# Performance work log

Measured on AMD Instinct MI355X. Metric: run time of the kernel, lower is better.

Reference implementation:

```python
import jax, jax.numpy as jnp
import numpy as np

# Architecture constants (from module defaults)
D, H, DH, P, G, DEPTH, M, NCLS = 192, 3, 64, 16, 14, 12, 128, 1000  # M = feature_map_dim // 2
EXITS = (4, 8, 12)
TEMP = 1.0 / np.sqrt(DH)  # Favor softmax_temp = 1/sqrt(d_head)
EPS_ATTN = 1e-6           # fast_transformers LinearAttention eps
LN_EPS = 1e-5


def ln(x, g, b):
    mu = x.mean(-1, keepdims=True)
    var = ((x - mu) ** 2).mean(-1, keepdims=True)
    return (x - mu) * jax.lax.rsqrt(var + LN_EPS) * g + b


def favor(x, omega):
    # FAVOR+ positive random features for the softmax kernel.
    # x: [B,L,H,DH], omega: [DH,M] -> phi: [B,L,H,2M]
    xs = x * np.float32(np.sqrt(TEMP))
    off = 0.5 * (xs * xs).sum(-1, keepdims=True)
    u = jnp.einsum('blhd,dm->blhm', xs, omega)
    phi = jnp.concatenate([jnp.exp(u - off), jnp.exp(-u - off)], axis=-1)
    return phi * np.float32(1.0 / np.sqrt(2 * M))


def forward(x, patch_w, patch_b, pe_ln_g, pe_ln_b, cls_token, pos_embed,
            Wq, bq, Wk, bk, Wv, bv, Wo, bo,
            ln1_g, ln1_b, ln2_g, ln2_b, lnb_g, lnb_b,
            W1, b1, W2, b2, omega, head_w, head_b):
    B = x.shape[0]
    # Patch embedding: Conv2d(k=16, s=16) == blocked einsum
    xp = x.reshape(B, 3, G, P, G, P)
    tok = jnp.einsum('bchpwq,dcpq->bhwd', xp, patch_w).reshape(B, G * G, D) + patch_b
    tok = ln(tok, pe_ln_g, pe_ln_b)  # PatchEmbed.norm (norm_layer=LayerNorm)
    tok = jnp.concatenate([jnp.broadcast_to(cls_token, (B, 1, D)), tok], axis=1) + pos_embed
    xc = tok  # [B, 197, D]
    outs = []
    for i in range(DEPTH):
        # --- linear (FAVOR) attention ---
        q = (xc @ Wq[i].T + bq[i]).reshape(B, -1, H, DH)
        k = (xc @ Wk[i].T + bk[i]).reshape(B, -1, H, DH)
        v = (xc @ Wv[i].T + bv[i]).reshape(B, -1, H, DH)
        Qp = favor(q, omega[i])
        Kp = favor(k, omega[i])
        KV = jnp.einsum('bshm,bshd->bhmd', Kp, v)
        Z = 1.0 / (jnp.einsum('blhm,bhm->blh', Qp, Kp.sum(axis=1)) + EPS_ATTN)
        attn = jnp.einsum('blhm,bhmd,blh->blhd', Qp, KV, Z).reshape(B, -1, D)
        # fast_transformers TransformerEncoderLayer (post-norm style)
        xc = xc + attn @ Wo[i].T + bo[i]
        y = xc = ln(xc, ln1_g[i], ln1_b[i])
        y = jax.nn.relu(y @ W1[i].T + b1[i]) @ W2[i].T + b2[i]
        xc = ln(xc + y, ln2_g[i], ln2_b[i])
        # per-block TransformerEncoder final norm (builder final_normalization)
        xc = ln(xc, lnb_g[i], lnb_b[i])
        if (i + 1) in EXITS:
            j = EXITS.index(i + 1)
            z = xc.mean(axis=1)  # AdaptiveAvgPool1d(1) over sequence
            outs.append(z @ head_w[j].T + head_b[j])
    return tuple(outs)


def setup_inputs() -> dict:
    key = jax.random.key(0)
    ks = iter(jax.random.split(key, 32))
    n = lambda shape, s=0.02: jax.random.normal(next(ks), shape, jnp.float32) * s
    return dict(
        x=jax.random.normal(next(ks), (64, 3, 224, 224), jnp.float32),
        patch_w=n((D, 3, P, P)), patch_b=jnp.zeros((D,), jnp.float32),
        pe_ln_g=jnp.ones((D,), jnp.float32), pe_ln_b=jnp.zeros((D,), jnp.float32),
        cls_token=n((1, 1, D)), pos_embed=n((1, G * G + 1, D)),
        Wq=n((DEPTH, D, D)), bq=jnp.zeros((DEPTH, D), jnp.float32),
        Wk=n((DEPTH, D, D)), bk=jnp.zeros((DEPTH, D), jnp.float32),
        Wv=n((DEPTH, D, D)), bv=jnp.zeros((DEPTH, D), jnp.float32),
        Wo=n((DEPTH, D, D)), bo=jnp.zeros((DEPTH, D), jnp.float32),
        ln1_g=jnp.ones((DEPTH, D), jnp.float32), ln1_b=jnp.zeros((DEPTH, D), jnp.float32),
        ln2_g=jnp.ones((DEPTH, D), jnp.float32), ln2_b=jnp.zeros((DEPTH, D), jnp.float32),
        lnb_g=jnp.ones((DEPTH, D), jnp.float32), lnb_b=jnp.zeros((DEPTH, D), jnp.float32),
        W1=n((DEPTH, 4 * D, D)), b1=jnp.zeros((DEPTH, 4 * D), jnp.float32),
        W2=n((DEPTH, D, 4 * D)), b2=jnp.zeros((DEPTH, D), jnp.float32),
        omega=jax.random.normal(next(ks), (DEPTH, DH, M), jnp.float32),
        head_w=n((len(EXITS), NCLS, D)), head_b=jnp.zeros((len(EXITS), NCLS), jnp.float32),
    )


def reference(x, patch_w, patch_b, pe_ln_g, pe_ln_b, cls_token, pos_embed,
              Wq, bq, Wk, bk, Wv, bv, Wo, bo,
              ln1_g, ln1_b, ln2_g, ln2_b, lnb_g, lnb_b,
              W1, b1, W2, b2, omega, head_w, head_b):
    return forward(x, patch_w, patch_b, pe_ln_g, pe_ln_b, cls_token, pos_embed,
                   Wq, bq, Wk, bk, Wv, bv, Wo, bo,
                   ln1_g, ln1_b, ln2_g, ln2_b, lnb_g, lnb_b,
                   W1, b1, W2, b2, omega, head_w, head_b)
```

## Files before the change

### kernel.cpp

```cpp
#include <hip/hip_runtime.h>
#include <math.h>

#define BB     64
#define LLEN   197
#define BLROWS 12608
#define MPAD   12672
#define DMODEL 192
#define NHEAD  3
#define DHEAD  64
#define M2FEAT 256
#define FFDIM  768
#define NDEPTH 12
#define NCLS   1000
#define NPATCH 196
#define BPROWS 12544
#define KPATCH 768
#define PHIRS  264
#define PHTRS  40
#define VLT    208

#define MODE_PLAIN 0
#define MODE_RELU  1
#define MODE_QKV   2

typedef unsigned short ushort;
typedef __attribute__((ext_vector_type(8))) short bf16x8;
typedef __attribute__((ext_vector_type(4))) float floatx4;
typedef __attribute__((ext_vector_type(4))) short short4v;

__device__ __forceinline__ float wave_reduce_sum(float v) {
#pragma unroll
  for (int s = 32; s > 0; s >>= 1) v += __shfl_xor(v, s, 64);
  return v;
}
__device__ __forceinline__ ushort f2bf(float f) {
  unsigned u = __float_as_uint(f);
  return (ushort)((u + 0x7fffu + ((u >> 16) & 1u)) >> 16);
}
__device__ __forceinline__ float bf2f(ushort u) {
  return __uint_as_float(((unsigned)u) << 16);
}
__device__ __forceinline__ void gll16(const ushort* g, ushort* l) {
  __builtin_amdgcn_global_load_lds(
      (const __attribute__((address_space(1))) void*)g,
      (__attribute__((address_space(3))) void*)l, 16, 0, 0);
}

__global__ void zero_buf(uint4* __restrict__ p, int n16) {
  const int i = blockIdx.x * 256 + threadIdx.x;
  if (i < n16) p[i] = uint4{0, 0, 0, 0};
}

__global__ __launch_bounds__(256) void gemm_bf2(
    const ushort* __restrict__ A, int lda,
    const ushort* __restrict__ W, int ldw,
    const float* __restrict__ bias,
    ushort* __restrict__ C, int ldc, ushort* __restrict__ Vt,
    int Kdim, int mode)
{
  __shared__ __align__(16) ushort As[2][128 * 64];
  __shared__ __align__(16) ushort Ws[2][64 * 64];
  const int tid = threadIdx.x;
  const int bm = blockIdx.x, bn = blockIdx.y;
  const int wave = tid >> 6, lane = tid & 63;
  const int wm = (wave >> 1) * 64, wn = (wave & 1) * 32;
  const int quad = lane >> 4, l16 = lane & 15;
  const int srow = lane >> 3;
  const int scol = ((lane & 7) ^ srow) * 8;
  const ushort* Ap = A + (size_t)(bm * 128) * lda;
  const ushort* Wp = W + (size_t)(bn * 64) * ldw;
  floatx4 acc[4][2] = {};
  const int nT = Kdim >> 6;
#pragma unroll
  for (int t = 0; t < 4; ++t) {
    const int rb = (t * 4 + wave) * 8;
    gll16(Ap + (size_t)(rb + srow) * lda + scol, &As[0][rb * 64]);
  }
#pragma unroll
  for (int t = 0; t < 2; ++t) {
    const int rb = (t * 4 + wave) * 8;
    gll16(Wp + (size_t)(rb + srow) * ldw + scol, &Ws[0][rb * 64]);
  }
  for (int kt = 0; kt < nT; ++kt) {
    const int cur = kt & 1;
    __syncthreads();
    if (kt + 1 < nT) {
      const int kk = (kt + 1) * 64, nxt = cur ^ 1;
#pragma unroll
      for (int t = 0; t < 4; ++t) {
        const int rb = (t * 4 + wave) * 8;
        gll16(Ap + (size_t)(rb + srow) * lda + kk + scol, &As[nxt][rb * 64]);
      }
#pragma unroll
      for (int t = 0; t < 2; ++t) {
        const int rb = (t * 4 + wave) * 8;
        gll16(Wp + (size_t)(rb + srow) * ldw + kk + scol, &Ws[nxt][rb * 64]);
      }
    }
#pragma unroll
    for (int ks = 0; ks < 2; ++ks) {
      bf16x8 af[4], bf[2];
#pragma unroll
      for (int i = 0; i < 4; ++i) {
        const int ra = wm + i * 16 + l16;
        af[i] = *(const bf16x8*)&As[cur][ra * 64 + ((((ks << 2) | quad) ^ (ra & 7)) * 8)];
      }
#pragma unroll
      for (int j = 0; j < 2; ++j) {
        const int rw = wn + j * 16 + l16;
        bf[j] = *(const bf16x8*)&Ws[cur][rw * 64 + ((((ks << 2) | quad) ^ (rw & 7)) * 8)];
      }
#pragma unroll
      for (int i = 0; i < 4; ++i)
#pragma unroll
        for (int j = 0; j < 2; ++j)
          acc[i][j] = __builtin_amdgcn_mfma_f32_16x16x32_bf16(af[i], bf[j], acc[i][j], 0, 0, 0);
    }
  }
  if (mode == MODE_QKV) {
#pragma unroll
    for (int i = 0; i < 4; ++i)
#pragma unroll
      for (int r = 0; r < 4; ++r) {
        const int grow = bm * 128 + wm + i * 16 + quad * 4 + r;
        const int bidx = grow / 197;
        const int lloc = grow - bidx * 197;
#pragma unroll
        for (int j = 0; j < 2; ++j) {
          const int col = bn * 64 + wn + j * 16 + l16;
          const float o = acc[i][j][r] + bias[col];
          if (col < 384) {
            C[(size_t)grow * ldc + col] = f2bf(o);
          } else if (grow < BLROWS) {
            const int h = (col - 384) >> 6, d = (col - 384) & 63;
            Vt[((size_t)(bidx * 3 + h) * 64 + d) * VLT + lloc] = f2bf(o);
          }
        }
      }
  } else {
#pragma unroll
    for (int j = 0; j < 2; ++j) {
      const int col = bn * 64 + wn + j * 16 + l16;
      const float bv = bias[col];
#pragma unroll
      for (int i = 0; i < 4; ++i)
#pragma unroll
        for (int r = 0; r < 4; ++r) {
          const int grow = bm * 128 + wm + i * 16 + quad * 4 + r;
          float o = acc[i][j][r] + bv;
          if (mode == MODE_RELU) o = fmaxf(o, 0.f);
          C[(size_t)grow * ldc + col] = f2bf(o);
        }
    }
  }
}

__global__ __launch_bounds__(256) void gemm_ln(
    const ushort* __restrict__ A, int lda,
    const ushort* __restrict__ W, int ldw,
    const float* __restrict__ bias,
    ushort* __restrict__ XC,
    const float* __restrict__ ga, const float* __restrict__ ba,
    const float* __restrict__ gb, const float* __restrict__ bb,
    int Kdim, int dln)
{
  __shared__ __align__(16) ushort As[2][32 * 64];
  __shared__ __align__(16) ushort Ws[2][192 * 64];
  __shared__ float p1s[2][32], p1q[2][32], p2s[2][32], p2q[2][32];
  const int tid = threadIdx.x;
  const int bm = blockIdx.x;
  const int wave = tid >> 6, lane = tid & 63;
  const int rg = wave >> 1, cg = wave & 1;
  const int quad = lane >> 4, l16 = lane & 15;
  const int srow = lane >> 3;
  const int scol = ((lane & 7) ^ srow) * 8;
  const ushort* Ap = A + (size_t)(bm * 32) * lda;
  floatx4 acc[6] = {};
  const int nT = Kdim >> 6;
  gll16(Ap + (size_t)(wave * 8 + srow) * lda + scol, &As[0][wave * 8 * 64]);
#pragma unroll
  for (int t = 0; t < 6; ++t) {
    const int rb = (t * 4 + wave) * 8;
    gll16(W + (size_t)(rb + srow) * ldw + scol, &Ws[0][rb * 64]);
  }
  for (int kt = 0; kt < nT; ++kt) {
    const int cur = kt & 1;
    __syncthreads();
    if (kt + 1 < nT) {
      const int kk = (kt + 1) * 64, nxt = cur ^ 1;
      gll16(Ap + (size_t)(wave * 8 + srow) * lda + kk + scol, &As[nxt][wave * 8 * 64]);
#pragma unroll
      for (int t = 0; t < 6; ++t) {
        const int rb = (t * 4 + wave) * 8;
        gll16(W + (size_t)(rb + srow) * ldw + kk + scol, &Ws[nxt][rb * 64]);
      }
    }
#pragma unroll
    for (int ks = 0; ks < 2; ++ks) {
      const int ra = rg * 16 + l16;
      const bf16x8 af = *(const bf16x8*)&As[cur][ra * 64 + ((((ks << 2) | quad) ^ (ra & 7)) * 8)];
#pragma unroll
      for (int j = 0; j < 6; ++j) {
        const int rw = (cg * 6 + j) * 16 + l16;
        const bf16x8 bf = *(const bf16x8*)&Ws[cur][rw * 64 + ((((ks << 2) | quad) ^ (rw & 7)) * 8)];
        acc[j] = __builtin_amdgcn_mfma_f32_16x16x32_bf16(af, bf, acc[j], 0, 0, 0);
      }
    }
  }
  float xr[4][6];
#pragma unroll
  for (int r = 0; r < 4; ++r) {
    const int rloc = rg * 16 + quad * 4 + r;
    const int row = bm * 32 + rloc;
    const ushort* xp = XC + (size_t)row * DMODEL;
    float s = 0.f, sq = 0.f;
#pragma unroll
    for (int j = 0; j < 6; ++j) {
      const int col = (cg * 6 + j) * 16 + l16;
      const float o = acc[j][r] + bias[col] + bf2f(xp[col]);
      xr[r][j] = o; s += o; sq += o * o;
    }
#pragma unroll
    for (int m = 1; m < 16; m <<= 1) {
      s += __shfl_xor(s, m, 64); sq += __shfl_xor(sq, m, 64);
    }
    if (l16 == 0) { p1s[cg][rloc] = s; p1q[cg][rloc] = sq; }
  }
  __syncthreads();
#pragma unroll
  for (int r = 0; r < 4; ++r) {
    const int rloc = rg * 16 + quad * 4 + r;
    const float s = p1s[0][rloc] + p1s[1][rloc];
    const float sq = p1q[0][rloc] + p1q[1][rloc];
    const float mu = s * (1.f / 192.f);
    const float var = sq * (1.f / 192.f) - mu * mu;
    const float rs = rsqrtf(var + 1e-5f);
#pragma unroll
    for (int j = 0; j < 6; ++j) {
      const int col = (cg * 6 + j) * 16 + l16;
      xr[r][j] = (xr[r][j] - mu) * rs * ga[col] + ba[col];
    }
  }
  if (dln) {
#pragma unroll
    for (int r = 0; r < 4; ++r) {
      const int rloc = rg * 16 + quad * 4 + r;
      float s = 0.f, sq = 0.f;
#pragma unroll
      for (int j = 0; j < 6; ++j) { s += xr[r][j]; sq += xr[r][j] * xr[r][j]; }
#pragma unroll
      for (int m = 1; m < 16; m <<= 1) {
        s += __shfl_xor(s, m, 64); sq += __shfl_xor(sq, m, 64);
      }
      if (l16 == 0) { p2s[cg][rloc] = s; p2q[cg][rloc] = sq; }
    }
    __syncthreads();
#pragma unroll
    for (int r = 0; r < 4; ++r) {
      const int rloc = rg * 16 + quad * 4 + r;
      const float s = p2s[0][rloc] + p2s[1][rloc];
      const float sq = p2q[0][rloc] + p2q[1][rloc];
      const float mu = s * (1.f / 192.f);
      const float var = sq * (1.f / 192.f) - mu * mu;
      const float rs = rsqrtf(var + 1e-5f);
#pragma unroll
      for (int j = 0; j < 6; ++j) {
        const int col = (cg * 6 + j) * 16 + l16;
        xr[r][j] = (xr[r][j] - mu) * rs * gb[col] + bb[col];
      }
    }
  }
#pragma unroll
  for (int r = 0; r < 4; ++r) {
    const int row = bm * 32 + rg * 16 + quad * 4 + r;
    ushort* xp = XC + (size_t)row * DMODEL;
#pragma unroll
    for (int j = 0; j < 6; ++j) xp[(cg * 6 + j) * 16 + l16] = f2bf(xr[r][j]);
  }
}

__global__ __launch_bounds__(256) void kv_fused(
    const ushort* __restrict__ qkv, const ushort* __restrict__ OmT,
    const ushort* __restrict__ Vt, ushort* __restrict__ KVt)
{
  __shared__ __align__(16) ushort Ks[32 * 64];
  __shared__ __align__(16) ushort Om[64 * 64];
  __shared__ __align__(16) ushort PhT[128 * PHTRS];
  __shared__ __align__(16) ushort Vts[2][64 * 32];
  __shared__ __align__(16) ushort Vcst[16 * 32];
  __shared__ float offs[32];
  const int tid = threadIdx.x;
  const int bh = blockIdx.x, mh = blockIdx.y;
  const int b = bh / 3, h = bh - b * 3;
  const int wave = tid >> 6, lane = tid & 63;
  const int quad = lane >> 4, l16 = lane & 15;
  const int lr8 = lane >> 3, g8 = lane & 7;
  const int lr4 = lane >> 2, g4 = lane & 3;
#pragma unroll
  for (int t = 0; t < 2; ++t) {
    const int rb = (t * 4 + wave) * 8;
    const int row = rb + lr8;
    gll16(OmT + (size_t)(mh * 64 + row) * 64 + ((g8 ^ (row & 7)) * 8), &Om[rb * 64]);
  }
  {
    const int rowK = wave * 8 + lr8;
    gll16(qkv + (size_t)(b * 197 + rowK) * 576 + 192 + h * 64 + ((g8 ^ (rowK & 7)) * 8),
          &Ks[wave * 8 * 64]);
    const int rowV = wave * 16 + lr4;
    gll16(Vt + ((size_t)bh * 64 + rowV) * VLT + ((g4 ^ (rowV & 3)) * 8),
          &Vts[0][wave * 16 * 32]);
  }
  for (int e = tid; e < 16 * 32; e += 256) Vcst[e] = (e < 32) ? 0x3F80 : 0;
  floatx4 acc[2][5] = {};
  for (int c = 0; c < 7; ++c) {
    const int l0 = c * 32;
    const int cur = c & 1;
    __syncthreads();
    if (tid < 64) {
      const int row = tid >> 1, half = tid & 1;
      float s = 0.f;
#pragma unroll
      for (int t = 0; t < 4; ++t) {
        bf16x8 v8 = *(const bf16x8*)&Ks[row * 64 + (((half * 4 + t) ^ (row & 7)) * 8)];
#pragma unroll
        for (int q = 0; q < 8; ++q) { float xv = bf2f((ushort)v8[q]); s += xv * xv; }
      }
      s += __shfl_xor(s, 1, 64);
      if (half == 0) offs[row] = 0.0625f * s;
    }
    floatx4 ui[2] = {};
#pragma unroll
    for (int ksb = 0; ksb < 2; ++ksb) {
      bf16x8 af[2], bfm;
#pragma unroll
      for (int i = 0; i < 2; ++i) {
        const int row = i * 16 + l16;
        af[i] = *(const bf16x8*)&Ks[row * 64 + (((quad + (ksb << 2)) ^ (row & 7)) * 8)];
      }
      {
        const int row = wave * 16 + l16;
        bfm = *(const bf16x8*)&Om[row * 64 + (((quad + (ksb << 2)) ^ (row & 7)) * 8)];
      }
#pragma unroll
      for (int i = 0; i < 2; ++i)
        ui[i] = __builtin_amdgcn_mfma_f32_16x16x32_bf16(af[i], bfm, ui[i], 0, 0, 0);
    }
    __syncthreads();
    {
      const int mloc = wave * 16 + l16;
#pragma unroll
      for (int i = 0; i < 2; ++i) {
#pragma unroll
        for (int r = 0; r < 4; ++r) {
          const int ll = i * 16 + quad * 4 + r;
          float ep = 0.f, em = 0.f;
          if (l0 + ll < 197) {
            const float off = offs[ll];
            const float u = ui[i][r];
            ep = __expf(u - off) * 0.0625f;
            em = __expf(-u - off) * 0.0625f;
          }
          PhT[mloc * PHTRS + ll] = f2bf(ep);
          PhT[(64 + mloc) * PHTRS + ll] = f2bf(em);
        }
      }
    }
    if (c + 1 < 7) {
      const int rowK = wave * 8 + lr8;
      const int lK = (c + 1) * 32 + rowK;
      gll16(qkv + (size_t)(b * 197 + lK) * 576 + 192 + h * 64 + ((g8 ^ (rowK & 7)) * 8),
            &Ks[wave * 8 * 64]);
      const int rowV = wave * 16 + lr4;
      gll16(Vt + ((size_t)bh * 64 + rowV) * VLT + (c + 1) * 32 + ((g4 ^ (rowV & 3)) * 8),
            &Vts[cur ^ 1][wave * 16 * 32]);
    }
    __syncthreads();
    bf16x8 af[2], bf[5];
#pragma unroll
    for (int i = 0; i < 2; ++i)
      af[i] = *(const bf16x8*)&PhT[(wave * 32 + i * 16 + l16) * PHTRS + quad * 8];
#pragma unroll
    for (int j = 0; j < 4; ++j) {
      const int row = j * 16 + l16;
      bf[j] = *(const bf16x8*)&Vts[cur][row * 32 + ((quad ^ (row & 3)) * 8)];
    }
    bf[4] = *(const bf16x8*)&Vcst[l16 * 32 + quad * 8];
#pragma unroll
    for (int i = 0; i < 2; ++i)
#pragma unroll
      for (int j = 0; j < 5; ++j)
        acc[i][j] = __builtin_amdgcn_mfma_f32_16x16x32_bf16(af[i], bf[j], acc[i][j], 0, 0, 0);
  }
#pragma unroll
  for (int i = 0; i < 2; ++i) {
    const int prow0 = wave * 32 + i * 16 + quad * 4;
    const int f0 = (prow0 < 64) ? (mh * 64 + prow0) : (128 + mh * 64 + prow0 - 64);
#pragma unroll
    for (int j = 0; j < 5; ++j) {
      const int d = j * 16 + l16;
      short4v pk;
#pragma unroll
      for (int r = 0; r < 4; ++r) pk[r] = (short)f2bf(acc[i][j][r]);
      *(short4v*)(KVt + ((size_t)bh * 80 + d) * 256 + f0) = pk;
    }
  }
}

__global__ __launch_bounds__(256) void attn_fused(
    const ushort* __restrict__ qkv, const ushort* __restrict__ OmT,
    const ushort* __restrict__ KVt, ushort* __restrict__ OUT)
{
  __shared__ __align__(16) ushort Phi[64 * PHIRS];
  __shared__ __align__(16) ushort Bs[2][80 * 32];
  __shared__ float offs[64];
  __shared__ float zs[64];
  ushort* Qs = Phi;
  ushort* Om = Phi + 64 * 64;
  const int tid = threadIdx.x;
  const int bx = blockIdx.x, bh = blockIdx.y;
  const int b = bh / 3, h = bh - b * 3;
  const int wave = tid >> 6, lane = tid & 63;
  const int quad = lane >> 4, l16 = lane & 15;
  const int lr8 = lane >> 3, g8 = lane & 7;
  const int lr4 = lane >> 2, g4 = lane & 3;
#pragma unroll
  for (int t = 0; t < 2; ++t) {
    const int rb = wave * 16 + t * 8;
    const int row = rb + lr8;
    const int l = bx * 64 + row;
    gll16(qkv + (size_t)(b * 197 + l) * 576 + h * 64 + ((g8 ^ (row & 7)) * 8), &Qs[rb * 64]);
  }
#pragma unroll
  for (int t = 0; t < 4; ++t) {
    const int rb = wave * 32 + t * 8;
    const int row = rb + lr8;
    gll16(OmT + (size_t)row * 64 + ((g8 ^ (row & 7)) * 8), &Om[rb * 64]);
  }
  __syncthreads();
  if (tid < 128) {
    const int row = tid >> 1, half = tid & 1;
    float s = 0.f;
#pragma unroll
    for (int t = 0; t < 4; ++t) {
      bf16x8 v8 = *(const bf16x8*)&Qs[row * 64 + (((half * 4 + t) ^ (row & 7)) * 8)];
#pragma unroll
      for (int q = 0; q < 8; ++q) { float xv = bf2f((ushort)v8[q]); s += xv * xv; }
    }
    s += __shfl_xor(s, 1, 64);
    if (half == 0) offs[row] = 0.0625f * s;
  }
  floatx4 uacc[8] = {};
#pragma unroll
  for (int ksb = 0; ksb < 2; ++ksb) {
    bf16x8 af, bf[8];
    {
      const int row = wave * 16 + l16;
      af = *(const bf16x8*)&Qs[row * 64 + (((quad + (ksb << 2)) ^ (row & 7)) * 8)];
    }
#pragma unroll
    for (int j = 0; j < 8; ++j) {
      const int row = j * 16 + l16;
      bf[j] = *(const bf16x8*)&Om[row * 64 + (((quad + (ksb << 2)) ^ (row & 7)) * 8)];
    }
#pragma unroll
    for (int j = 0; j < 8; ++j)
      uacc[j] = __builtin_amdgcn_mfma_f32_16x16x32_bf16(af, bf[j], uacc[j], 0, 0, 0);
  }
  __syncthreads();
#pragma unroll
  for (int r = 0; r < 4; ++r) {
    const int l = wave * 16 + quad * 4 + r;
    const float off = offs[l];
#pragma unroll
    for (int j = 0; j < 8; ++j) {
      const int m = j * 16 + l16;
      const float u = uacc[j][r];
      Phi[l * PHIRS + m]       = f2bf(__expf(u - off)  * 0.0625f);
      Phi[l * PHIRS + m + 128] = f2bf(__expf(-u - off) * 0.0625f);
    }
  }
  const ushort* Bp = KVt + (size_t)bh * 80 * 256;
  {
    const int row = wave * 16 + lr4;
    gll16(Bp + (size_t)row * 256 + ((g4 ^ (row & 3)) * 8), &Bs[0][wave * 16 * 32]);
    if (wave == 0)
      gll16(Bp + (size_t)(64 + lr4) * 256 + ((g4 ^ (lr4 & 3)) * 8), &Bs[0][64 * 32]);
  }
  floatx4 acc[5] = {};
  for (int c = 0; c < 8; ++c) {
    const int cur = c & 1;
    __syncthreads();
    if (c + 1 < 8) {
      const int m0 = (c + 1) * 32, nxt = cur ^ 1;
      const int row = wave * 16 + lr4;
      gll16(Bp + (size_t)row * 256 + m0 + ((g4 ^ (row & 3)) * 8), &Bs[nxt][wave * 16 * 32]);
      if (wave == 0)
        gll16(Bp + (size_t)(64 + lr4) * 256 + m0 + ((g4 ^ (lr4 & 3)) * 8), &Bs[nxt][64 * 32]);
    }
    const int m0 = c * 32;
    bf16x8 af, bf[5];
    af = *(const bf16x8*)&Phi[(wave * 16 + l16) * PHIRS + m0 + quad * 8];
#pragma unroll
    for (int j = 0; j < 5; ++j) {
      const int row = j * 16 + l16;
      bf[j] = *(const bf16x8*)&Bs[cur][row * 32 + ((quad ^ (row & 3)) * 8)];
    }
#pragma unroll
    for (int j = 0; j < 5; ++j)
      acc[j] = __builtin_amdgcn_mfma_f32_16x16x32_bf16(af, bf[j], acc[j], 0, 0, 0);
  }
  if (l16 == 0) {
#pragma unroll
    for (int r = 0; r < 4; ++r)
      zs[wave * 16 + quad * 4 + r] = acc[4][r];
  }
  __syncthreads();
#pragma unroll
  for (int r = 0; r < 4; ++r) {
    const int ll = wave * 16 + quad * 4 + r;
    const int l = bx * 64 + ll;
    if (l >= 197) continue;
    const float z = 1.f / (zs[ll] + 1e-6f);
#pragma unroll
    for (int j = 0; j < 4; ++j)
      OUT[(size_t)(b * 197 + l) * 192 + h * 64 + j * 16 + l16] =
          f2bf(acc[j][r] * z);
  }
}

__global__ void conv_qkv(const float* __restrict__ Wq, const float* __restrict__ Wk,
                         const float* __restrict__ Wv, const float* __restrict__ bq,
                         const float* __restrict__ bk, const float* __restrict__ bv,
                         ushort* __restrict__ dst, float* __restrict__ bdst) {
  const int l = blockIdx.y;
  const int e = blockIdx.x * 256 + threadIdx.x;
  const int n = e / 192, k = e - n * 192;
  const float* src;
  if (n < 192)      src = Wq + (size_t)l * 36864 + n * 192;
  else if (n < 384) src = Wk + (size_t)l * 36864 + (n - 192) * 192;
  else              src = Wv + (size_t)l * 36864 + (n - 384) * 192;
  dst[(size_t)l * 640 * 192 + e] = f2bf(src[k]);
  if (e < 576) {
    float bvv;
    if (e < 192)      bvv = bq[l * 192 + e];
    else if (e < 384) bvv = bk[l * 192 + e - 192];
    else              bvv = bv[l * 192 + e - 384];
    bdst[l * 576 + e] = bvv;
  }
}

__global__ void conv_pad(const float* __restrict__ src, ushort* __restrict__ dst,
                         int NK, int padNK) {
  const int l = blockIdx.y;
  const int e = blockIdx.x * 256 + threadIdx.x;
  if (e < NK) dst[(size_t)l * padNK + e] = f2bf(src[(size_t)l * NK + e]);
}

__global__ void conv_omt(const float* __restrict__ om, ushort* __restrict__ dst) {
  const int l = blockIdx.y;
  const int e = blockIdx.x * 256 + threadIdx.x;
  const int m = e >> 6, d = e & 63;
  dst[(size_t)l * 8192 + e] = f2bf(0.35355339059327379f * om[(size_t)l * 8192 + d * 128 + m]);
}

__global__ __launch_bounds__(256) void im2col_kernel(
    const float* __restrict__ X, ushort* __restrict__ Apd)
{
  const int bp = blockIdx.x;
  const int b = bp / NPATCH, p = bp - b * NPATCH;
  const int gh = p / 14, gw = p - gh * 14;
  for (int e = threadIdx.x; e < KPATCH; e += 256) {
    const int c = e >> 8, rem = e & 255, ph = rem >> 4, pw = rem & 15;
    Apd[(size_t)bp * KPATCH + e] =
        f2bf(X[((size_t)(b * 3 + c) * 224 + gh * 16 + ph) * 224 + gw * 16 + pw]);
  }
}

__global__ __launch_bounds__(256) void assemble_kernel(
    const ushort* __restrict__ TK, const float* __restrict__ g,
    const float* __restrict__ bt, const float* __restrict__ cls,
    const float* __restrict__ pos, ushort* __restrict__ XC)
{
  const int w = threadIdx.x >> 6, lane = threadIdx.x & 63;
  const int row = blockIdx.x * 4 + w;
  const int b = row / LLEN, l = row - b * LLEN;
  float o0, o1, o2;
  if (l == 0) {
    o0 = cls[lane]; o1 = cls[lane + 64]; o2 = cls[lane + 128];
  } else {
    const ushort* tp = TK + (size_t)(b * NPATCH + l - 1) * DMODEL;
    const float x0 = bf2f(tp[lane]), x1 = bf2f(tp[lane + 64]), x2 = bf2f(tp[lane + 128]);
    const float s  = wave_reduce_sum(x0 + x1 + x2);
    const float sq = wave_reduce_sum(x0 * x0 + x1 * x1 + x2 * x2);
    const float mu = s * (1.f / 192.f);
    const float var = sq * (1.f / 192.f) - mu * mu;
    const float rs = rsqrtf(var + 1e-5f);
    o0 = (x0 - mu) * rs * g[lane]       + bt[lane];
    o1 = (x1 - mu) * rs * g[lane + 64]  + bt[lane + 64];
    o2 = (x2 - mu) * rs * g[lane + 128] + bt[lane + 128];
  }
  o0 += pos[l * DMODEL + lane];
  o1 += pos[l * DMODEL + lane + 64];
  o2 += pos[l * DMODEL + lane + 128];
  ushort* xp = XC + (size_t)row * DMODEL;
  xp[lane] = f2bf(o0); xp[lane + 64] = f2bf(o1); xp[lane + 128] = f2bf(o2);
}

__global__ __launch_bounds__(256) void head_kernel(
    const ushort* __restrict__ XC, const float* __restrict__ HW,
    const float* __restrict__ HB, float* __restrict__ OUTp)
{
  __shared__ float zsh[DMODEL];
  const int b = blockIdx.y;
  const int tid = threadIdx.x;
  const int wave = tid >> 6, lane = tid & 63;
  if (wave < 3) {
    const int d = wave * 64 + lane;
    const ushort* xp = XC + (size_t)b * LLEN * DMODEL + d;
    float s = 0.f;
#pragma unroll 4
    for (int l = 0; l < LLEN; ++l) s += bf2f(xp[(size_t)l * DMODEL]);
    zsh[d] = s * (1.f / 197.f);
  }
  __syncthreads();
  const int n = blockIdx.x * 256 + tid;
  if (n < NCLS) {
    const float* w = HW + (size_t)n * DMODEL;
    float s = HB[n];
#pragma unroll 4
    for (int d = 0; d < DMODEL; ++d) s = fmaf(zsh[d], w[d], s);
    OUTp[(size_t)b * NCLS + n] = s;
  }
}

extern "C" void kernel_launch(void* const* d_in, const int* in_sizes, int n_in,
                              void* d_out, int out_size, void* d_ws, size_t ws_size,
                              hipStream_t stream) {
  const float* x        = (const float*)d_in[0];
  const float* patch_w  = (const float*)d_in[1];
  const float* patch_b  = (const float*)d_in[2];
  const float* pe_ln_g  = (const float*)d_in[3];
  const float* pe_ln_b  = (const float*)d_in[4];
  const float* cls_tok  = (const float*)d_in[5];
  const float* pos_emb  = (const float*)d_in[6];
  const float* Wq = (const float*)d_in[7];
  const float* bq = (const float*)d_in[8];
  const float* Wk = (const float*)d_in[9];
  const float* bk = (const float*)d_in[10];
  const float* Wv = (const float*)d_in[11];
  const float* bv = (const float*)d_in[12];
  const float* Wo = (const float*)d_in[13];
  const float* bo = (const float*)d_in[14];
  const float* ln1_g = (const float*)d_in[15];
  const float* ln1_b = (const float*)d_in[16];
  const float* ln2_g = (const float*)d_in[17];
  const float* ln2_b = (const float*)d_in[18];
  const float* lnb_g = (const float*)d_in[19];
  const float* lnb_b = (const float*)d_in[20];
  const float* W1 = (const float*)d_in[21];
  const float* b1 = (const float*)d_in[22];
  const float* W2 = (const float*)d_in[23];
  const float* b2 = (const float*)d_in[24];
  const float* omega  = (const float*)d_in[25];
  const float* head_w = (const float*)d_in[26];
  const float* head_b = (const float*)d_in[27];
  float* out = (float*)d_out;
  char* wsb = (char*)d_ws;

  size_t off = 0;
  auto carve = [&](size_t bytes) { size_t o = off; off += (bytes + 255) & ~(size_t)255; return o; };
  ushort* xc     = (ushort*)(wsb + carve((size_t)MPAD * 192 * 2));
  ushort* qkv    = (ushort*)(wsb + carve((size_t)MPAD * 576 * 2));
  ushort* ab     = (ushort*)(wsb + carve((size_t)MPAD * 192 * 2));
  ushort* hidden = (ushort*)(wsb + carve((size_t)MPAD * 768 * 2));
  ushort* KVt    = (ushort*)(wsb + carve((size_t)192 * 80 * 256 * 2));
  ushort* Vt     = (ushort*)(wsb + carve((size_t)192 * 64 * VLT * 2 + 1024));
  float*  bqkv   = (float*)(wsb + carve((size_t)12 * 576 * 4));
  ushort* Wqkv_bf = (ushort*)(wsb + carve((size_t)12 * 640 * 192 * 2));
  ushort* Wo_bf   = (ushort*)(wsb + carve((size_t)12 * 256 * 192 * 2));
  ushort* W1_bf   = (ushort*)(wsb + carve((size_t)12 * 768 * 192 * 2));
  ushort* W2_bf   = (ushort*)(wsb + carve((size_t)12 * 256 * 768 * 2));
  ushort* Wp_bf   = (ushort*)(wsb + carve((size_t)256 * 768 * 2));
  ushort* Om_bf   = (ushort*)(wsb + carve((size_t)12 * 128 * 64 * 2));
  ushort* i2c     = hidden;

  {
    const int n16 = (int)(((size_t)192 * 64 * VLT * 2 + 1024) / 16);
    zero_buf<<<(n16 + 255) / 256, 256, 0, stream>>>((uint4*)Vt, n16);
  }

  conv_qkv<<<dim3(432, 12), 256, 0, stream>>>(Wq, Wk, Wv, bq, bk, bv, Wqkv_bf, bqkv);
  conv_pad<<<dim3(144, 12), 256, 0, stream>>>(Wo, Wo_bf, 36864, 256 * 192);
  conv_pad<<<dim3(576, 12), 256, 0, stream>>>(W1, W1_bf, 147456, 768 * 192);
  conv_pad<<<dim3(576, 12), 256, 0, stream>>>(W2, W2_bf, 147456, 256 * 768);
  conv_pad<<<dim3(576, 1), 256, 0, stream>>>(patch_w, Wp_bf, 147456, 256 * 768);
  conv_omt<<<dim3(32, 12), 256, 0, stream>>>(omega, Om_bf);

  im2col_kernel<<<BPROWS, 256, 0, stream>>>(x, i2c);
  gemm_bf2<<<dim3(98, 3), 256, 0, stream>>>(i2c, KPATCH, Wp_bf, KPATCH,
      patch_b, ab, DMODEL, nullptr, KPATCH, MODE_PLAIN);
  assemble_kernel<<<BLROWS / 4, 256, 0, stream>>>(ab, pe_ln_g, pe_ln_b,
                                                  cls_tok, pos_emb, xc);

  const int exits[3] = {3, 7, 11};
  for (int i = 0; i < NDEPTH; ++i) {
    gemm_bf2<<<dim3(99, 9), 256, 0, stream>>>(xc, DMODEL,
        Wqkv_bf + (size_t)i * 640 * 192, DMODEL, bqkv + i * 576,
        qkv, 576, Vt, DMODEL, MODE_QKV);
    kv_fused<<<dim3(192, 2), 256, 0, stream>>>(qkv,
        Om_bf + (size_t)i * 8192, Vt, KVt);
    attn_fused<<<dim3(4, 192), 256, 0, stream>>>(qkv,
        Om_bf + (size_t)i * 8192, KVt, ab);
    gemm_ln<<<MPAD / 32, 256, 0, stream>>>(ab, DMODEL,
        Wo_bf + (size_t)i * 256 * 192, DMODEL, bo + i * DMODEL, xc,
        ln1_g + i * DMODEL, ln1_b + i * DMODEL, nullptr, nullptr,
        DMODEL, 0);
    gemm_bf2<<<dim3(99, 12), 256, 0, stream>>>(xc, DMODEL,
        W1_bf + (size_t)i * 768 * 192, DMODEL, b1 + i * FFDIM,
        hidden, FFDIM, nullptr, DMODEL, MODE_RELU);
    gemm_ln<<<MPAD / 32, 256, 0, stream>>>(hidden, FFDIM,
        W2_bf + (size_t)i * 256 * 768, FFDIM, b2 + i * DMODEL, xc,
        ln2_g + i * DMODEL, ln2_b + i * DMODEL,
        lnb_g + i * DMODEL, lnb_b + i * DMODEL,
        FFDIM, 1);

    for (int j = 0; j < 3; ++j) {
      if (i == exits[j]) {
        head_kernel<<<dim3(4, BB), 256, 0, stream>>>(
            xc, head_w + (size_t)j * NCLS * DMODEL, head_b + (size_t)j * NCLS,
            out + (size_t)j * BB * NCLS);
      }
    }
  }
}
```

Baseline: 1.322 ms.

## Load GEMM weight fragments directly into registers and halve LN-GEMM row tile

Both GEMM kernels stop staging weight tiles in LDS and instead load the B-operand MFMA fragments straight from global memory into registers, prefetching the next k-tile while computing. The fused GEMM+LayerNorm kernel also drops to 16 rows per block with each wave owning 48 columns, which doubles the grid and reduces LDS use, raising occupancy. The cost is more global (L2) weight traffic per block, uncoalesced 16-byte row loads, and register pressure from double-buffered fragments.

```diff
diff --git a/kernel.cpp b/kernel.cpp
--- a/kernel.cpp
+++ b/kernel.cpp
@@ -59,7 +59,6 @@
     int Kdim, int mode)
 {
   __shared__ __align__(16) ushort As[2][128 * 64];
-  __shared__ __align__(16) ushort Ws[2][64 * 64];
   const int tid = threadIdx.x;
   const int bm = blockIdx.x, bn = blockIdx.y;
   const int wave = tid >> 6, lane = tid & 63;
@@ -68,7 +67,8 @@
   const int srow = lane >> 3;
   const int scol = ((lane & 7) ^ srow) * 8;
   const ushort* Ap = A + (size_t)(bm * 128) * lda;
-  const ushort* Wp = W + (size_t)(bn * 64) * ldw;
+  const ushort* Wp0 = W + (size_t)(bn * 64 + wn + l16) * ldw;
+  const ushort* Wp1 = W + (size_t)(bn * 64 + wn + 16 + l16) * ldw;
   floatx4 acc[4][2] = {};
   const int nT = Kdim >> 6;
 #pragma unroll
@@ -76,14 +76,16 @@
     const int rb = (t * 4 + wave) * 8;
     gll16(Ap + (size_t)(rb + srow) * lda + scol, &As[0][rb * 64]);
   }
-#pragma unroll
-  for (int t = 0; t < 2; ++t) {
-    const int rb = (t * 4 + wave) * 8;
-    gll16(Wp + (size_t)(rb + srow) * ldw + scol, &Ws[0][rb * 64]);
+  bf16x8 wf[2][2];
+#pragma unroll
+  for (int ks = 0; ks < 2; ++ks) {
+    wf[ks][0] = *(const bf16x8*)(Wp0 + (ks * 4 + quad) * 8);
+    wf[ks][1] = *(const bf16x8*)(Wp1 + (ks * 4 + quad) * 8);
   }
   for (int kt = 0; kt < nT; ++kt) {
     const int cur = kt & 1;
     __syncthreads();
+    bf16x8 wfn[2][2];
     if (kt + 1 < nT) {
       const int kk = (kt + 1) * 64, nxt = cur ^ 1;
 #pragma unroll
@@ -92,29 +94,30 @@
         gll16(Ap + (size_t)(rb + srow) * lda + kk + scol, &As[nxt][rb * 64]);
       }
 #pragma unroll
-      for (int t = 0; t < 2; ++t) {
-        const int rb = (t * 4 + wave) * 8;
-        gll16(Wp + (size_t)(rb + srow) * ldw + kk + scol, &Ws[nxt][rb * 64]);
+      for (int ks = 0; ks < 2; ++ks) {
+        wfn[ks][0] = *(const bf16x8*)(Wp0 + kk + (ks * 4 + quad) * 8);
+        wfn[ks][1] = *(const bf16x8*)(Wp1 + kk + (ks * 4 + quad) * 8);
       }
     }
 #pragma unroll
     for (int ks = 0; ks < 2; ++ks) {
-      bf16x8 af[4], bf[2];
+      bf16x8 af[4];
 #pragma unroll
       for (int i = 0; i < 4; ++i) {
         const int ra = wm + i * 16 + l16;
         af[i] = *(const bf16x8*)&As[cur][ra * 64 + ((((ks << 2) | quad) ^ (ra & 7)) * 8)];
       }
 #pragma unroll
-      for (int j = 0; j < 2; ++j) {
-        const int rw = wn + j * 16 + l16;
-        bf[j] = *(const bf16x8*)&Ws[cur][rw * 64 + ((((ks << 2) | quad) ^ (rw & 7)) * 8)];
-      }
-#pragma unroll
       for (int i = 0; i < 4; ++i)
 #pragma unroll
         for (int j = 0; j < 2; ++j)
-          acc[i][j] = __builtin_amdgcn_mfma_f32_16x16x32_bf16(af[i], bf[j], acc[i][j], 0, 0, 0);
+          acc[i][j] = __builtin_amdgcn_mfma_f32_16x16x32_bf16(af[i], wf[ks][j], acc[i][j], 0, 0, 0);
+    }
+    if (kt + 1 < nT) {
+#pragma unroll
+      for (int ks = 0; ks < 2; ++ks)
+#pragma unroll
+        for (int j = 0; j < 2; ++j) wf[ks][j] = wfn[ks][j];
     }
   }
   if (mode == MODE_QKV) {
@@ -164,59 +167,68 @@
     const float* __restrict__ gb, const float* __restrict__ bb,
     int Kdim, int dln)
 {
-  __shared__ __align__(16) ushort As[2][32 * 64];
-  __shared__ __align__(16) ushort Ws[2][192 * 64];
-  __shared__ float p1s[2][32], p1q[2][32], p2s[2][32], p2q[2][32];
+  __shared__ __align__(16) ushort As[2][16 * 64];
+  __shared__ float p1s[4][16], p1q[4][16], p2s[4][16], p2q[4][16];
   const int tid = threadIdx.x;
   const int bm = blockIdx.x;
   const int wave = tid >> 6, lane = tid & 63;
-  const int rg = wave >> 1, cg = wave & 1;
   const int quad = lane >> 4, l16 = lane & 15;
   const int srow = lane >> 3;
   const int scol = ((lane & 7) ^ srow) * 8;
-  const ushort* Ap = A + (size_t)(bm * 32) * lda;
-  floatx4 acc[6] = {};
+  const ushort* Ap = A + (size_t)(bm * 16) * lda;
+  const ushort* Wp0 = W + (size_t)((wave * 3 + 0) * 16 + l16) * ldw;
+  const ushort* Wp1 = W + (size_t)((wave * 3 + 1) * 16 + l16) * ldw;
+  const ushort* Wp2 = W + (size_t)((wave * 3 + 2) * 16 + l16) * ldw;
+  floatx4 acc[3] = {};
   const int nT = Kdim >> 6;
-  gll16(Ap + (size_t)(wave * 8 + srow) * lda + scol, &As[0][wave * 8 * 64]);
-#pragma unroll
-  for (int t = 0; t < 6; ++t) {
-    const int rb = (t * 4 + wave) * 8;
-    gll16(W + (size_t)(rb + srow) * ldw + scol, &Ws[0][rb * 64]);
+  if (wave < 2) gll16(Ap + (size_t)(wave * 8 + srow) * lda + scol, &As[0][wave * 8 * 64]);
+  bf16x8 wf[2][3];
+#pragma unroll
+  for (int ks = 0; ks < 2; ++ks) {
+    wf[ks][0] = *(const bf16x8*)(Wp0 + (ks * 4 + quad) * 8);
+    wf[ks][1] = *(const bf16x8*)(Wp1 + (ks * 4 + quad) * 8);
+    wf[ks][2] = *(const bf16x8*)(Wp2 + (ks * 4 + quad) * 8);
   }
   for (int kt = 0; kt < nT; ++kt) {
     const int cur = kt & 1;
     __syncthreads();
+    bf16x8 wfn[2][3];
     if (kt + 1 < nT) {
       const int kk = (kt + 1) * 64, nxt = cur ^ 1;
-      gll16(Ap + (size_t)(wave * 8 + srow) * lda + kk + scol, &As[nxt][wave * 8 * 64]);
-#pragma unroll
-      for (int t = 0; t < 6; ++t) {
-        const int rb = (t * 4 + wave) * 8;
-        gll16(W + (size_t)(rb + srow) * ldw + kk + scol, &Ws[nxt][rb * 64]);
+      if (wave < 2)
+        gll16(Ap + (size_t)(wave * 8 + srow) * lda + kk + scol, &As[nxt][wave * 8 * 64]);
+#pragma unroll
+      for (int ks = 0; ks < 2; ++ks) {
+        wfn[ks][0] = *(const bf16x8*)(Wp0 + kk + (ks * 4 + quad) * 8);
+        wfn[ks][1] = *(const bf16x8*)(Wp1 + kk + (ks * 4 + quad) * 8);
+        wfn[ks][2] = *(const bf16x8*)(Wp2 + kk + (ks * 4 + quad) * 8);
       }
     }
 #pragma unroll
     for (int ks = 0; ks < 2; ++ks) {
-      const int ra = rg * 16 + l16;
+      const int ra = l16;
       const bf16x8 af = *(const bf16x8*)&As[cur][ra * 64 + ((((ks << 2) | quad) ^ (ra & 7)) * 8)];
 #pragma unroll
-      for (int j = 0; j < 6; ++j) {
-        const int rw = (cg * 6 + j) * 16 + l16;
-        const bf16x8 bf = *(const bf16x8*)&Ws[cur][rw * 64 + ((((ks << 2) | quad) ^ (rw & 7)) * 8)];
-        acc[j] = __builtin_amdgcn_mfma_f32_16x16x32_bf16(af, bf, acc[j], 0, 0, 0);
-      }
-    }
-  }
-  float xr[4][6];
+      for (int j = 0; j < 3; ++j)
+        acc[j] = __builtin_amdgcn_mfma_f32_16x16x32_bf16(af, wf[ks][j], acc[j], 0, 0, 0);
+    }
+    if (kt + 1 < nT) {
+#pragma unroll
+      for (int ks = 0; ks < 2; ++ks)
+#pragma unroll
+        for (int j = 0; j < 3; ++j) wf[ks][j] = wfn[ks][j];
+    }
+  }
+  float xr[4][3];
 #pragma unroll
   for (int r = 0; r < 4; ++r) {
-    const int rloc = rg * 16 + quad * 4 + r;
-    const int row = bm * 32 + rloc;
+    const int rloc = quad * 4 + r;
+    const int row = bm * 16 + rloc;
     const ushort* xp = XC + (size_t)row * DMODEL;
     float s = 0.f, sq = 0.f;
 #pragma unroll
-    for (int j = 0; j < 6; ++j) {
-      const int col = (cg * 6 + j) * 16 + l16;
+    for (int j = 0; j < 3; ++j) {
+      const int col = (wave * 3 + j) * 16 + l16;
       const float o = acc[j][r] + bias[col] + bf2f(xp[col]);
       xr[r][j] = o; s += o; sq += o * o;
     }
@@ -224,58 +236,58 @@
     for (int m = 1; m < 16; m <<= 1) {
       s += __shfl_xor(s, m, 64); sq += __shfl_xor(sq, m, 64);
     }
-    if (l16 == 0) { p1s[cg][rloc] = s; p1q[cg][rloc] = sq; }
+    if (l16 == 0) { p1s[wave][rloc] = s; p1q[wave][rloc] = sq; }
   }
   __syncthreads();
 #pragma unroll
   for (int r = 0; r < 4; ++r) {
-    const int rloc = rg * 16 + quad * 4 + r;
-    const float s = p1s[0][rloc] + p1s[1][rloc];
-    const float sq = p1q[0][rloc] + p1q[1][rloc];
+    const int rloc = quad * 4 + r;
+    const float s = p1s[0][rloc] + p1s[1][rloc] + p1s[2][rloc] + p1s[3][rloc];
+    const float sq = p1q[0][rloc] + p1q[1][rloc] + p1q[2][rloc] + p1q[3][rloc];
     const float mu = s * (1.f / 192.f);
     const float var = sq * (1.f / 192.f) - mu * mu;
     const float rs = rsqrtf(var + 1e-5f);
 #pragma unroll
-    for (int j = 0; j < 6; ++j) {
-      const int col = (cg * 6 + j) * 16 + l16;
+    for (int j = 0; j < 3; ++j) {
+      const int col = (wave * 3 + j) * 16 + l16;
       xr[r][j] = (xr[r][j] - mu) * rs * ga[col] + ba[col];
     }
   }
   if (dln) {
 #pragma unroll
     for (int r = 0; r < 4; ++r) {
-      const int rloc = rg * 16 + quad * 4 + r;
+      const int rloc = quad * 4 + r;
       float s = 0.f, sq = 0.f;
 #pragma unroll
-      for (int j = 0; j < 6; ++j) { s += xr[r][j]; sq += xr[r][j] * xr[r][j]; }
+      for (int j = 0; j < 3; ++j) { s += xr[r][j]; sq += xr[r][j] * xr[r][j]; }
 #pragma unroll
       for (int m = 1; m < 16; m <<= 1) {
         s += __shfl_xor(s, m, 64); sq += __shfl_xor(sq, m, 64);
       }
-      if (l16 == 0) { p2s[cg][rloc] = s; p2q[cg][rloc] = sq; }
+      if (l16 == 0) { p2s[wave][rloc] = s; p2q[wave][rloc] = sq; }
     }
     __syncthreads();
 #pragma unroll
     for (int r = 0; r < 4; ++r) {
-      const int rloc = rg * 16 + quad * 4 + r;
-      const float s = p2s[0][rloc] + p2s[1][rloc];
-      const float sq = p2q[0][rloc] + p2q[1][rloc];
+      const int rloc = quad * 4 + r;
+      const float s = p2s[0][rloc] + p2s[1][rloc] + p2s[2][rloc] + p2s[3][rloc];
+      const float sq = p2q[0][rloc] + p2q[1][rloc] + p2q[2][rloc] + p2q[3][rloc];
       const float mu = s * (1.f / 192.f);
       const float var = sq * (1.f / 192.f) - mu * mu;
       const float rs = rsqrtf(var + 1e-5f);
 #pragma unroll
-      for (int j = 0; j < 6; ++j) {
-        const int col = (cg * 6 + j) * 16 + l16;
+      for (int j = 0; j < 3; ++j) {
+        const int col = (wave * 3 + j) * 16 + l16;
         xr[r][j] = (xr[r][j] - mu) * rs * gb[col] + bb[col];
       }
     }
   }
 #pragma unroll
   for (int r = 0; r < 4; ++r) {
-    const int row = bm * 32 + rg * 16 + quad * 4 + r;
+    const int row = bm * 16 + quad * 4 + r;
     ushort* xp = XC + (size_t)row * DMODEL;
 #pragma unroll
-    for (int j = 0; j < 6; ++j) xp[(cg * 6 + j) * 16 + l16] = f2bf(xr[r][j]);
+    for (int j = 0; j < 3; ++j) xp[(wave * 3 + j) * 16 + l16] = f2bf(xr[r][j]);
   }
 }
 
@@ -711,14 +723,14 @@
         Om_bf + (size_t)i * 8192, Vt, KVt);
     attn_fused<<<dim3(4, 192), 256, 0, stream>>>(qkv,
         Om_bf + (size_t)i * 8192, KVt, ab);
-    gemm_ln<<<MPAD / 32, 256, 0, stream>>>(ab, DMODEL,
+    gemm_ln<<<MPAD / 16, 256, 0, stream>>>(ab, DMODEL,
         Wo_bf + (size_t)i * 256 * 192, DMODEL, bo + i * DMODEL, xc,
         ln1_g + i * DMODEL, ln1_b + i * DMODEL, nullptr, nullptr,
         DMODEL, 0);
     gemm_bf2<<<dim3(99, 12), 256, 0, stream>>>(xc, DMODEL,
         W1_bf + (size_t)i * 768 * 192, DMODEL, b1 + i * FFDIM,
         hidden, FFDIM, nullptr, DMODEL, MODE_RELU);
-    gemm_ln<<<MPAD / 32, 256, 0, stream>>>(hidden, FFDIM,
+    gemm_ln<<<MPAD / 16, 256, 0, stream>>>(hidden, FFDIM,
         W2_bf + (size_t)i * 256 * 768, FFDIM, b2 + i * DMODEL, xc,
         ln2_g + i * DMODEL, ln2_b + i * DMODEL,
         lnb_g + i * DMODEL, lnb_b + i * DMODEL,
```

Result: slower. 1.698 ms (+28.4%).
